# Kernel optimization log

Measured on AMD Instinct MI355X. Metric: run time of the kernel, lower is better.

Reference implementation:

```python
import jax, jax.numpy as jnp
import numpy as np

N = 10000        # nodes
E = 160000       # graph edges (avg degree 16)
EI = 100000      # interaction edges
EP = 50000       # positive interaction edges
EA = 50000       # a2b edges
H, D = 4, 128    # GAT heads, per-head (and per-layer) dim
F_IN, F_EDGE = 39, 27   # 17+19+3 node feats, 27 edge feats
EMB = 256
FCN_IN = F_IN + 3 * D + D  # 551: x stacked with 3 GAT outputs + GCN output

PARAM_SHAPES = []
for l, fin in enumerate([F_IN, D, D]):
    PARAM_SHAPES += [(f"gat{l}_W", (fin, H * D)), (f"gat{l}_We", (F_EDGE, H * D)),
                     (f"gat{l}_asrc", (H, D)), (f"gat{l}_adst", (H, D)),
                     (f"gat{l}_aedge", (H, D)), (f"gat{l}_b", (D,))]
PARAM_SHAPES += [("gcn_W", (D, D)), ("gcn_b", (D,))]
for nm, fi, hh, fo in [("fcn", FCN_IN, 1024, EMB), ("link", 2 * EMB + 2, 1024, 1),
                       ("a2b", 2 * EMB, 1024, 6), ("node", EMB, 1024, 16),
                       ("int", 2 * EMB + 2, 1024, 3)]:
    PARAM_SHAPES += [(f"{nm}_W1", (fi, hh)), (f"{nm}_b1", (hh,)),
                     (f"{nm}_g", (hh,)), (f"{nm}_be", (hh,)),
                     (f"{nm}_W2", (hh, fo)), (f"{nm}_b2", (fo,))]
PARAM_NAMES = [n for n, _ in PARAM_SHAPES]


def setup_inputs():
    ks = jax.random.split(jax.random.key(0), len(PARAM_SHAPES) + 10)
    inp = {
        "x": jax.random.normal(ks[0], (N, F_IN), jnp.float32),
        "edge_index": jax.random.randint(ks[1], (2, E), 0, N),
        "edge_attr": jax.random.normal(ks[2], (E, F_EDGE), jnp.float32),
        "interaction_edge_index_pos": jax.random.randint(ks[3], (2, EP), 0, N),
        "interaction_edge_index": jax.random.randint(ks[4], (2, EI), 0, N),
        "xyz_data": jax.random.normal(ks[5], (N, 3), jnp.float32),
        "vector_data": jax.random.normal(ks[6], (N, 3), jnp.float32),
        "a2b_index": jax.random.randint(ks[7], (2, EA), 0, N),
        "mask": jnp.zeros((1,), jnp.float32),  # only used by the (disabled) evolver path
    }
    for i, (name, shp) in enumerate(PARAM_SHAPES):
        if name.endswith("_g"):
            inp[name] = jnp.ones(shp, jnp.float32)        # BatchNorm gamma
        elif name.endswith(("_be", "_b", "_b1", "_b2")):
            inp[name] = jnp.zeros(shp, jnp.float32)       # biases / BN beta
        else:
            inp[name] = jax.random.normal(ks[10 + i], shp, jnp.float32) * 0.05
    return inp


def _bn(h, g, b, eps=1e-5):
    # BatchNorm1d in training mode: biased batch statistics over axis 0
    m = h.mean(0)
    v = ((h - m) ** 2).mean(0)
    return (h - m) * jax.lax.rsqrt(v + eps) * g + b


def _seg_softmax(logits, seg, n):
    m = jax.ops.segment_max(logits, seg, num_segments=n)
    e = jnp.exp(logits - m[seg])
    s = jax.ops.segment_sum(e, seg, num_segments=n)
    return e / (s[seg] + 1e-16)


def _cos(a, b, eps=1e-8):
    na = jnp.maximum(jnp.sqrt((a * a).sum(1)), eps)
    nb = jnp.maximum(jnp.sqrt((b * b).sum(1)), eps)
    return (a * b).sum(1) / (na * nb)


def _forward(x, edge_attr, xyz_data, vector_data, edge_index, iep, iei, a2b_index, params):
    p = dict(zip(PARAM_NAMES, params))
    n = x.shape[0]
    src, dst = edge_index[0], edge_index[1]
    loops = jnp.arange(n)
    # GATConv add_self_loops with fill_value='mean': per-node mean of incoming edge_attr
    cnt = jax.ops.segment_sum(jnp.ones(src.shape[0], x.dtype), dst, num_segments=n)
    loop_attr = jax.ops.segment_sum(edge_attr, dst, num_segments=n) / jnp.maximum(cnt, 1.0)[:, None]
    src_a = jnp.concatenate([src, loops])
    dst_a = jnp.concatenate([dst, loops])
    ea_a = jnp.concatenate([edge_attr, loop_attr], 0)

    def gat(xx, W, We, asrc, adst, aedge, b):
        h = (xx @ W).reshape(n, H, D)
        a_s = (h * asrc).sum(-1)                               # [n,H]
        a_d = (h * adst).sum(-1)                               # [n,H]
        a_e = ((ea_a @ We).reshape(-1, H, D) * aedge).sum(-1)  # [E',H]
        alpha = jax.nn.leaky_relu(a_s[src_a] + a_d[dst_a] + a_e, 0.2)
        alpha = _seg_softmax(alpha, dst_a, n)                  # softmax over incoming edges
        out = jax.ops.segment_sum(h[src_a] * alpha[:, :, None], dst_a, num_segments=n)
        return out.mean(1) + b                                 # concat=False -> mean over heads

    out = x
    steps = [x]
    for l in range(3):
        out = jax.nn.relu(gat(out, p[f"gat{l}_W"], p[f"gat{l}_We"], p[f"gat{l}_asrc"],
                              p[f"gat{l}_adst"], p[f"gat{l}_aedge"], p[f"gat{l}_b"]))
        steps.append(out)
    # GCNConv: self loops (weight 1) + symmetric normalization
    deg = jax.ops.segment_sum(jnp.ones(dst_a.shape[0], x.dtype), dst_a, num_segments=n)
    dinv = jnp.where(deg > 0, deg ** -0.5, 0.0)
    norm = dinv[src_a] * dinv[dst_a]
    hg = out @ p["gcn_W"]
    out = jax.ops.segment_sum(hg[src_a] * norm[:, None], dst_a, num_segments=n) + p["gcn_b"]
    steps.append(out)

    feat = jnp.concatenate(steps, 1)                           # [n, 551]
    h = jax.nn.relu(feat @ p["fcn_W1"] + p["fcn_b1"])
    h = _bn(h, p["fcn_g"], p["fcn_be"])
    emb = jax.nn.relu(h @ p["fcn_W2"] + p["fcn_b2"])           # [n, 256]

    def head(z, nm):
        hh = jax.nn.relu(z @ p[f"{nm}_W1"] + p[f"{nm}_b1"])
        hh = _bn(hh, p[f"{nm}_g"], p[f"{nm}_be"])
        return hh @ p[f"{nm}_W2"] + p[f"{nm}_b2"]

    def pair_feat(idx):
        z = jnp.concatenate([emb[idx[0]], emb[idx[1]]], 1)
        d = ((xyz_data[idx[0]] - xyz_data[idx[1]]) ** 2).sum(1)  # squared distance (no sqrt)
        a = _cos(vector_data[idx[0]], vector_data[idx[1]])
        return jnp.concatenate([z, d[:, None], a[:, None]], 1)

    link_preds = head(pair_feat(iei), "link")
    a2b_preds = head(jnp.concatenate([emb[a2b_index[0]], emb[a2b_index[1]]], 1), "a2b")
    node_preds = head(emb, "node")
    int_preds = head(pair_feat(iep), "int")
    return (link_preds, a2b_preds, node_preds, int_preds)


def reference(x, edge_index, edge_attr, interaction_edge_index_pos, interaction_edge_index,
              xyz_data, vector_data, a2b_index, mask,
              gat0_W, gat0_We, gat0_asrc, gat0_adst, gat0_aedge, gat0_b,
              gat1_W, gat1_We, gat1_asrc, gat1_adst, gat1_aedge, gat1_b,
              gat2_W, gat2_We, gat2_asrc, gat2_adst, gat2_aedge, gat2_b,
              gcn_W, gcn_b,
              fcn_W1, fcn_b1, fcn_g, fcn_be, fcn_W2, fcn_b2,
              link_W1, link_b1, link_g, link_be, link_W2, link_b2,
              a2b_W1, a2b_b1, a2b_g, a2b_be, a2b_W2, a2b_b2,
              node_W1, node_b1, node_g, node_be, node_W2, node_b2,
              int_W1, int_b1, int_g, int_be, int_W2, int_b2):
    loc = locals()
    params = tuple(loc[nm] for nm in PARAM_NAMES)
    return _forward(x, edge_attr, xyz_data, vector_data, edge_index,
                    interaction_edge_index_pos, interaction_edge_index, a2b_index, params)
```

## Files before the change

### kernel.cpp

```cpp
#include <hip/hip_runtime.h>
#include <hip/hip_bf16.h>
#include <cstdint>
#include <cstddef>

typedef __attribute__((ext_vector_type(8))) short bf16x8;
typedef __attribute__((ext_vector_type(4))) float f32x4;

__device__ inline float bf2f(unsigned short u) {
    union { float f; unsigned int i; } c; c.i = ((unsigned int)u) << 16; return c.f;
}
__device__ inline unsigned short f2b(float v) {
    __hip_bfloat16 h = __float2bfloat16(v);
    union { __hip_bfloat16 b; unsigned short u; } c; c.b = h; return c.u;
}

__device__ inline float wmax64(float v) {
    #pragma unroll
    for (int o = 32; o; o >>= 1) v = fmaxf(v, __shfl_xor(v, o));
    return v;
}
__device__ inline float wsum64(float v) {
    #pragma unroll
    for (int o = 32; o; o >>= 1) v += __shfl_xor(v, o);
    return v;
}

__global__ void k_count(const int* __restrict__ dst, int* __restrict__ indeg, int E_) {
    int e = blockIdx.x * 256 + threadIdx.x;
    if (e < E_) atomicAdd(&indeg[dst[e]], 1);
}

__global__ __launch_bounds__(1024) void k_scan(const int* __restrict__ indeg, int* __restrict__ coff, int nn) {
    __shared__ int part[1024];
    const int t = threadIdx.x;
    const int CH = (nn + 1023) >> 10;
    int loc[16];
    int s = 0;
    #pragma unroll
    for (int j = 0; j < 16; ++j) {
        if (j < CH) {
            int idx = t * CH + j;
            loc[j] = s;
            s += (idx < nn) ? indeg[idx] : 0;
        }
    }
    part[t] = s;
    __syncthreads();
    for (int o = 1; o < 1024; o <<= 1) {
        int v = (t >= o) ? part[t - o] : 0;
        __syncthreads();
        part[t] += v;
        __syncthreads();
    }
    const int base = (t > 0) ? part[t - 1] : 0;
    #pragma unroll
    for (int j = 0; j < 16; ++j) {
        if (j < CH) {
            int idx = t * CH + j;
            if (idx < nn) coff[idx] = base + loc[j];
        }
    }
    if (t == 1023) coff[nn] = part[1023];
}

__global__ void k_fill(const int* __restrict__ dst, const int* __restrict__ coff,
                       int* __restrict__ fill, int* __restrict__ ceid, int E_) {
    int e = blockIdx.x * 256 + threadIdx.x;
    if (e < E_) {
        int d = dst[e];
        int p = atomicAdd(&fill[d], 1);
        ceid[coff[d] + p] = e;
    }
}

__global__ void k_copy_x(const float* __restrict__ x, float* __restrict__ feat, int nn) {
    int t = blockIdx.x * 256 + threadIdx.x;
    if (t < nn * 39) feat[(size_t)(t / 39) * 551 + (t % 39)] = x[t];
}

__global__ __launch_bounds__(128) void k_loopattr(const float* __restrict__ ea, const int* __restrict__ coff,
                                                  const int* __restrict__ ceid, float* __restrict__ la, int nn) {
    int g = blockIdx.x * 4 + (threadIdx.x >> 5);
    int lane = threadIdx.x & 31;
    if (g >= nn || lane >= 27) return;
    int beg = coff[g], cnt = coff[g + 1] - beg;
    float v = 0.f;
    for (int e = 0; e < cnt; ++e) v += ea[(size_t)ceid[beg + e] * 27 + lane];
    la[(size_t)g * 27 + lane] = v / fmaxf((float)cnt, 1.f);
}

__global__ void k_wea(const float* __restrict__ We, const float* __restrict__ aedge, float* __restrict__ Wea) {
    int t = threadIdx.x;
    if (t >= 108) return;
    int f = t >> 2, hh = t & 3;
    float v = 0.f;
    for (int d = 0; d < 128; ++d) v += We[(size_t)f * 512 + hh * 128 + d] * aedge[hh * 128 + d];
    Wea[f * 4 + hh] = v;
}

__global__ void k_ae(const float* __restrict__ ea, const float* __restrict__ la,
                     const float* __restrict__ Wea, float* __restrict__ a_e, int E_, int nn) {
    int r = blockIdx.x * 256 + threadIdx.x;
    if (r >= E_ + nn) return;
    const float* src = (r < E_) ? (ea + (size_t)r * 27) : (la + (size_t)(r - E_) * 27);
    float o0 = 0, o1 = 0, o2 = 0, o3 = 0;
    #pragma unroll
    for (int f = 0; f < 27; ++f) {
        float xv = src[f];
        o0 += xv * Wea[f * 4 + 0];
        o1 += xv * Wea[f * 4 + 1];
        o2 += xv * Wea[f * 4 + 2];
        o3 += xv * Wea[f * 4 + 3];
    }
    a_e[(size_t)r * 4 + 0] = o0; a_e[(size_t)r * 4 + 1] = o1;
    a_e[(size_t)r * 4 + 2] = o2; a_e[(size_t)r * 4 + 3] = o3;
}

__global__ void k_asd(const float* __restrict__ h, const float* __restrict__ asrc,
                      const float* __restrict__ adst, float* __restrict__ a_s,
                      float* __restrict__ a_d, int nn) {
    int t = blockIdx.x * 256 + threadIdx.x;
    if (t >= nn * 4) return;
    int node = t >> 2, hh = t & 3;
    const float* hp = h + (size_t)node * 512 + hh * 128;
    float vs = 0.f, vd = 0.f;
    for (int d = 0; d < 128; ++d) {
        float xv = hp[d];
        vs += xv * asrc[hh * 128 + d];
        vd += xv * adst[hh * 128 + d];
    }
    a_s[t] = vs;
    a_d[t] = vd;
}

__global__ __launch_bounds__(64) void k_attn(
    const float* __restrict__ h, const float* __restrict__ a_s, const float* __restrict__ a_d,
    const float* __restrict__ a_e, const int* __restrict__ esrc,
    const int* __restrict__ coff, const int* __restrict__ ceid,
    const float* __restrict__ bvec, float* __restrict__ feat, int colofs, int E_) {
    const int i = blockIdx.x;
    const int lane = threadIdx.x;
    const int beg = coff[i];
    const int cnt = coff[i + 1] - beg;
    const int total = cnt + 1;
    const float d0 = a_d[i * 4 + 0], d1 = a_d[i * 4 + 1], d2 = a_d[i * 4 + 2], d3 = a_d[i * 4 + 3];
    float m0 = -1e30f, m1 = -1e30f, m2 = -1e30f, m3 = -1e30f;
    for (int e = lane; e < total; e += 64) {
        int eid, s;
        if (e < cnt) { eid = ceid[beg + e]; s = esrc[eid]; } else { eid = E_ + i; s = i; }
        float l0 = a_s[s * 4 + 0] + d0 + a_e[(size_t)eid * 4 + 0];
        float l1 = a_s[s * 4 + 1] + d1 + a_e[(size_t)eid * 4 + 1];
        float l2 = a_s[s * 4 + 2] + d2 + a_e[(size_t)eid * 4 + 2];
        float l3 = a_s[s * 4 + 3] + d3 + a_e[(size_t)eid * 4 + 3];
        l0 = l0 > 0.f ? l0 : 0.2f * l0;
        l1 = l1 > 0.f ? l1 : 0.2f * l1;
        l2 = l2 > 0.f ? l2 : 0.2f * l2;
        l3 = l3 > 0.f ? l3 : 0.2f * l3;
        m0 = fmaxf(m0, l0); m1 = fmaxf(m1, l1); m2 = fmaxf(m2, l2); m3 = fmaxf(m3, l3);
    }
    m0 = wmax64(m0); m1 = wmax64(m1); m2 = wmax64(m2); m3 = wmax64(m3);
    float s0 = 0, s1 = 0, s2 = 0, s3 = 0;
    for (int e = lane; e < total; e += 64) {
        int eid, s;
        if (e < cnt) { eid = ceid[beg + e]; s = esrc[eid]; } else { eid = E_ + i; s = i; }
        float l0 = a_s[s * 4 + 0] + d0 + a_e[(size_t)eid * 4 + 0];
        float l1 = a_s[s * 4 + 1] + d1 + a_e[(size_t)eid * 4 + 1];
        float l2 = a_s[s * 4 + 2] + d2 + a_e[(size_t)eid * 4 + 2];
        float l3 = a_s[s * 4 + 3] + d3 + a_e[(size_t)eid * 4 + 3];
        l0 = l0 > 0.f ? l0 : 0.2f * l0;
        l1 = l1 > 0.f ? l1 : 0.2f * l1;
        l2 = l2 > 0.f ? l2 : 0.2f * l2;
        l3 = l3 > 0.f ? l3 : 0.2f * l3;
        s0 += __expf(l0 - m0); s1 += __expf(l1 - m1);
        s2 += __expf(l2 - m2); s3 += __expf(l3 - m3);
    }
    s0 = wsum64(s0); s1 = wsum64(s1); s2 = wsum64(s2); s3 = wsum64(s3);
    const int myh = lane >> 4;
    const float mm = myh == 0 ? m0 : myh == 1 ? m1 : myh == 2 ? m2 : m3;
    const float sv = myh == 0 ? s0 : myh == 1 ? s1 : myh == 2 ? s2 : s3;
    const float dd = myh == 0 ? d0 : myh == 1 ? d1 : myh == 2 ? d2 : d3;
    const float iv = 1.f / (sv + 1e-16f);
    float acc[8] = {0, 0, 0, 0, 0, 0, 0, 0};
    for (int e = 0; e < total; ++e) {
        int eid, s;
        if (e < cnt) { eid = ceid[beg + e]; s = esrc[eid]; } else { eid = E_ + i; s = i; }
        float l = a_s[s * 4 + myh] + dd + a_e[(size_t)eid * 4 + myh];
        l = l > 0.f ? l : 0.2f * l;
        const float wgt = __expf(l - mm) * iv;
        const float4* hp = (const float4*)(h + (size_t)s * 512 + lane * 8);
        float4 x0 = hp[0], x1 = hp[1];
        acc[0] += wgt * x0.x; acc[1] += wgt * x0.y; acc[2] += wgt * x0.z; acc[3] += wgt * x0.w;
        acc[4] += wgt * x1.x; acc[5] += wgt * x1.y; acc[6] += wgt * x1.z; acc[7] += wgt * x1.w;
    }
    __shared__ float sh[512];
    #pragma unroll
    for (int j = 0; j < 8; ++j) sh[lane * 8 + j] = acc[j];
    __syncthreads();
    #pragma unroll
    for (int r = 0; r < 2; ++r) {
        int d = lane * 2 + r;
        float v = 0.25f * (sh[d] + sh[128 + d] + sh[256 + d] + sh[384 + d]) + bvec[d];
        feat[(size_t)i * 551 + colofs + d] = fmaxf(v, 0.f);
    }
}

__global__ __launch_bounds__(64) void k_gcn(const float* __restrict__ hg, const int* __restrict__ esrc,
    const int* __restrict__ coff, const int* __restrict__ ceid, const int* __restrict__ indeg,
    const float* __restrict__ bvec, float* __restrict__ feat) {
    const int i = blockIdx.x;
    const int lane = threadIdx.x;
    const int beg = coff[i];
    const int cnt = coff[i + 1] - beg;
    const float di = rsqrtf((float)(indeg[i] + 1));
    const int d = lane * 2;
    float acc0 = hg[(size_t)i * 128 + d] * di;
    float acc1 = hg[(size_t)i * 128 + d + 1] * di;
    for (int e = 0; e < cnt; ++e) {
        int eid = ceid[beg + e];
        int s = esrc[eid];
        float ds = rsqrtf((float)(indeg[s] + 1));
        acc0 += hg[(size_t)s * 128 + d] * ds;
        acc1 += hg[(size_t)s * 128 + d + 1] * ds;
    }
    feat[(size_t)i * 551 + 423 + d] = acc0 * di + bvec[d];
    feat[(size_t)i * 551 + 423 + d + 1] = acc1 * di + bvec[d + 1];
}

__global__ void k_pair(const int* __restrict__ idx, const float* __restrict__ xyz,
                       const float* __restrict__ vec, float* __restrict__ dv,
                       float* __restrict__ av, int P) {
    int p = blockIdx.x * 256 + threadIdx.x;
    if (p >= P) return;
    int i = idx[p], j = idx[P + p];
    float dx = xyz[i * 3] - xyz[j * 3];
    float dy = xyz[i * 3 + 1] - xyz[j * 3 + 1];
    float dz = xyz[i * 3 + 2] - xyz[j * 3 + 2];
    dv[p] = dx * dx + dy * dy + dz * dz;
    float a0 = vec[i * 3], a1 = vec[i * 3 + 1], a2 = vec[i * 3 + 2];
    float b0 = vec[j * 3], b1 = vec[j * 3 + 1], b2 = vec[j * 3 + 2];
    float na = fmaxf(sqrtf(a0 * a0 + a1 * a1 + a2 * a2), 1e-8f);
    float nb = fmaxf(sqrtf(b0 * b0 + b1 * b1 + b2 * b2), 1e-8f);
    av[p] = (a0 * b0 + a1 * b1 + a2 * b2) / (na * nb);
}

__global__ void k_stage_a(const float* __restrict__ src, int lds, int off,
                          unsigned short* __restrict__ dst, int ldd, int M, int K, int Mp) {
    int idx = blockIdx.x * 256 + threadIdx.x;
    if (idx >= Mp * ldd) return;
    int m = idx / ldd, k = idx - m * ldd;
    float v = (m < M && k < K) ? src[(size_t)m * lds + off + k] : 0.f;
    dst[idx] = f2b(v);
}

__global__ void k_conv_bt(const float* __restrict__ src, int ldn,
                          unsigned short* __restrict__ dst, int Kp, int K, int N, int Np) {
    int idx = blockIdx.x * 256 + threadIdx.x;
    if (idx >= Np * Kp) return;
    int nrow = idx / Kp, k = idx - nrow * Kp;
    float v = (nrow < N && k < K) ? src[(size_t)k * ldn + nrow] : 0.f;
    dst[idx] = f2b(v);
}

template<int OUT, bool RELU, bool BIAS>
__global__ __launch_bounds__(256) void gemm_mfma(
    const unsigned short* __restrict__ A, int lda,
    const unsigned short* __restrict__ Bt, int ldb,
    const float* __restrict__ bias,
    void* __restrict__ Cv, int ldc,
    int M, int N, int K) {
    const int t = threadIdx.x;
    const int lane = t & 63;
    const int wid = t >> 6;
    const int wm = wid >> 1, wn = wid & 1;
    const int bm0 = blockIdx.y * 128 + wm * 64;
    const int bn0 = blockIdx.x * 128 + wn * 64;
    const int r = lane & 15, g = lane >> 4;
    f32x4 acc[4][4] = {};
    const unsigned short* Ap = A + (size_t)(bm0 + r) * lda + 8 * g;
    const unsigned short* Bp = Bt + (size_t)(bn0 + r) * ldb + 8 * g;
    for (int k0 = 0; k0 < K; k0 += 32) {
        bf16x8 a[4], b[4];
        #pragma unroll
        for (int i = 0; i < 4; ++i) {
            a[i] = *(const bf16x8*)(Ap + (size_t)(i * 16) * lda + k0);
            b[i] = *(const bf16x8*)(Bp + (size_t)(i * 16) * ldb + k0);
        }
        #pragma unroll
        for (int i = 0; i < 4; ++i)
            #pragma unroll
            for (int j = 0; j < 4; ++j)
                acc[i][j] = __builtin_amdgcn_mfma_f32_16x16x32_bf16(a[i], b[j], acc[i][j], 0, 0, 0);
    }
    #pragma unroll
    for (int i = 0; i < 4; ++i) {
        #pragma unroll
        for (int reg = 0; reg < 4; ++reg) {
            const int row = bm0 + i * 16 + 4 * g + reg;
            if (row >= M) continue;
            #pragma unroll
            for (int j = 0; j < 4; ++j) {
                const int col = bn0 + j * 16 + r;
                if (col >= N) continue;
                float v = acc[i][j][reg];
                if constexpr (BIAS) v += bias[col];
                if constexpr (RELU) v = fmaxf(v, 0.f);
                if constexpr (OUT == 0) ((float*)Cv)[(size_t)row * ldc + col] = v;
                else ((unsigned short*)Cv)[(size_t)row * ldc + col] = f2b(v);
            }
        }
    }
}

__global__ __launch_bounds__(256) void k_stats1b(const unsigned short* __restrict__ Hm, int M, float* __restrict__ part) {
    const int b = blockIdx.x, t = threadIdx.x;
    const int chunk = (M + 255) / 256;
    const int r0 = b * chunk;
    const int r1 = min(M, r0 + chunk);
    float s[4] = {0, 0, 0, 0}, ss[4] = {0, 0, 0, 0};
    for (int r = r0; r < r1; ++r) {
        const ushort4 q = *(const ushort4*)(Hm + (size_t)r * 1024 + t * 4);
        float v0 = bf2f(q.x), v1 = bf2f(q.y), v2 = bf2f(q.z), v3 = bf2f(q.w);
        s[0] += v0; ss[0] += v0 * v0;
        s[1] += v1; ss[1] += v1 * v1;
        s[2] += v2; ss[2] += v2 * v2;
        s[3] += v3; ss[3] += v3 * v3;
    }
    #pragma unroll
    for (int j = 0; j < 4; ++j) {
        part[(size_t)b * 2048 + t * 4 + j] = s[j];
        part[(size_t)b * 2048 + 1024 + t * 4 + j] = ss[j];
    }
}

__global__ __launch_bounds__(256) void k_red1(const float* __restrict__ part, float* __restrict__ tmp,
                                              int NB, int nch) {
    const int c = blockIdx.x * 256 + threadIdx.x;
    const int ch = blockIdx.y;
    const int per = (NB + nch - 1) / nch;
    const int b0 = ch * per;
    const int b1 = min(NB, b0 + per);
    float s = 0.f;
    for (int b = b0; b < b1; ++b) s += part[(size_t)b * 2048 + c];
    tmp[(size_t)ch * 2048 + c] = s;
}
__global__ void k_red2(const float* __restrict__ tmp, float* __restrict__ mv, int M, int nch) {
    int c = blockIdx.x * 256 + threadIdx.x;
    if (c >= 1024) return;
    float s = 0.f, ss = 0.f;
    for (int ch = 0; ch < nch; ++ch) {
        s += tmp[(size_t)ch * 2048 + c];
        ss += tmp[(size_t)ch * 2048 + 1024 + c];
    }
    float m = s / (float)M;
    float v = ss / (float)M - m * m;
    mv[c] = m;
    mv[1024 + c] = fmaxf(v, 0.f);
}

__global__ __launch_bounds__(256) void k_fold(const float* __restrict__ W2, const float* __restrict__ g,
    const float* __restrict__ be, const float* __restrict__ b2, const float* __restrict__ mv,
    float* __restrict__ W2f, float* __restrict__ b2f, int NO) {
    const int c = blockIdx.x;
    const int t = threadIdx.x;
    __shared__ float red[256];
    float accb = 0.f;
    for (int k = t; k < 1024; k += 256) {
        float s = (1.f / sqrtf(mv[1024 + k] + 1e-5f)) * g[k];
        float wv = W2[(size_t)k * NO + c];
        W2f[(size_t)k * NO + c] = wv * s;
        accb += (be[k] - mv[k] * s) * wv;
    }
    red[t] = accb;
    __syncthreads();
    for (int o = 128; o; o >>= 1) {
        if (t < o) red[t] += red[t + o];
        __syncthreads();
    }
    if (t == 0) b2f[c] = b2[c] + red[0];
}

template<bool HASEX>
__global__ __launch_bounds__(256) void k_pairA(
    const unsigned short* __restrict__ u0, const unsigned short* __restrict__ u1,
    const float* __restrict__ b1, const float* __restrict__ W1ex,
    const int* __restrict__ idx, const float* __restrict__ dv, const float* __restrict__ av,
    int P, float* __restrict__ part) {
    const int b = blockIdx.x, t = threadIdx.x;
    const int chunk = (P + 1023) / 1024;
    const int r0 = b * chunk;
    const int r1 = min(P, r0 + chunk);
    const float4 bb = *(const float4*)(b1 + t * 4);
    float4 wd = make_float4(0, 0, 0, 0), wa = make_float4(0, 0, 0, 0);
    if constexpr (HASEX) {
        wd = *(const float4*)(W1ex + t * 4);
        wa = *(const float4*)(W1ex + 1024 + t * 4);
    }
    float s[4] = {0, 0, 0, 0}, ss[4] = {0, 0, 0, 0};
    for (int r = r0; r < r1; ++r) {
        const int i0 = idx[r], i1 = idx[P + r];
        const ushort4 q0 = *(const ushort4*)(u0 + (size_t)i0 * 1024 + t * 4);
        const ushort4 q1 = *(const ushort4*)(u1 + (size_t)i1 * 1024 + t * 4);
        float h[4];
        h[0] = bf2f(q0.x) + bf2f(q1.x) + bb.x;
        h[1] = bf2f(q0.y) + bf2f(q1.y) + bb.y;
        h[2] = bf2f(q0.z) + bf2f(q1.z) + bb.z;
        h[3] = bf2f(q0.w) + bf2f(q1.w) + bb.w;
        if constexpr (HASEX) {
            const float d = dv[r], a = av[r];
            h[0] += d * wd.x + a * wa.x;
            h[1] += d * wd.y + a * wa.y;
            h[2] += d * wd.z + a * wa.z;
            h[3] += d * wd.w + a * wa.w;
        }
        #pragma unroll
        for (int j = 0; j < 4; ++j) {
            float hv = fmaxf(h[j], 0.f);
            s[j] += hv; ss[j] += hv * hv;
        }
    }
    #pragma unroll
    for (int j = 0; j < 4; ++j) {
        part[(size_t)b * 2048 + t * 4 + j] = s[j];
        part[(size_t)b * 2048 + 1024 + t * 4 + j] = ss[j];
    }
}

template<int NO, bool HASEX>
__global__ __launch_bounds__(256) void k_pairB(
    const unsigned short* __restrict__ u0, const unsigned short* __restrict__ u1,
    const float* __restrict__ b1, const float* __restrict__ W1ex,
    const float* __restrict__ W2f, const float* __restrict__ b2f,
    const int* __restrict__ idx, const float* __restrict__ dv, const float* __restrict__ av,
    float* __restrict__ out, int P) {
    const int t = threadIdx.x;
    const int wid = t >> 6, lane = t & 63;
    const int row = blockIdx.x * 4 + wid;
    if (row >= P) return;
    const int i0 = idx[row], i1 = idx[P + row];
    const int k0 = lane * 16;
    float d = 0.f, a = 0.f;
    if constexpr (HASEX) { d = dv[row]; a = av[row]; }
    float acc[NO];
    #pragma unroll
    for (int no = 0; no < NO; ++no) acc[no] = 0.f;
    const unsigned short* p0 = u0 + (size_t)i0 * 1024 + k0;
    const unsigned short* p1 = u1 + (size_t)i1 * 1024 + k0;
    union { uint4 u; unsigned short us[8]; } qa0, qa1, qb0, qb1;
    qa0.u = *(const uint4*)(p0);
    qa1.u = *(const uint4*)(p0 + 8);
    qb0.u = *(const uint4*)(p1);
    qb1.u = *(const uint4*)(p1 + 8);
    #pragma unroll
    for (int j = 0; j < 16; ++j) {
        const int kk = k0 + j;
        float h = (j < 8 ? bf2f(qa0.us[j]) : bf2f(qa1.us[j - 8]))
                + (j < 8 ? bf2f(qb0.us[j]) : bf2f(qb1.us[j - 8]))
                + b1[kk];
        if constexpr (HASEX) h += d * W1ex[kk] + a * W1ex[1024 + kk];
        const float hv = fmaxf(h, 0.f);
        #pragma unroll
        for (int no = 0; no < NO; ++no) acc[no] += hv * W2f[(size_t)kk * NO + no];
    }
    #pragma unroll
    for (int no = 0; no < NO; ++no) {
        float v = acc[no];
        #pragma unroll
        for (int o = 32; o; o >>= 1) v += __shfl_down(v, o);
        if (lane == 0) out[(size_t)row * NO + no] = v + b2f[no];
    }
}

extern "C" void kernel_launch(void* const* d_in, const int* in_sizes, int n_in,
                              void* d_out, int out_size, void* d_ws, size_t ws_size,
                              hipStream_t stream) {
    (void)n_in; (void)out_size; (void)ws_size;
    const float* x     = (const float*)d_in[0];
    const int*   eidx  = (const int*)d_in[1];
    const float* eattr = (const float*)d_in[2];
    const int*   iep   = (const int*)d_in[3];
    const int*   iei   = (const int*)d_in[4];
    const float* xyz   = (const float*)d_in[5];
    const float* vecd  = (const float*)d_in[6];
    const int*   a2bi  = (const int*)d_in[7];

    const int n   = in_sizes[0] / 39;
    const int E_  = in_sizes[1] / 2;
    const int EPn = in_sizes[3] / 2;
    const int EIn = in_sizes[4] / 2;
    const int EAn = in_sizes[7] / 2;
    const int Mp  = (n + 127) & ~127;
    const int MB  = (n + 127) / 128;

    const float* gatW[3]  = {(const float*)d_in[9],  (const float*)d_in[15], (const float*)d_in[21]};
    const float* gatWe[3] = {(const float*)d_in[10], (const float*)d_in[16], (const float*)d_in[22]};
    const float* gatAs[3] = {(const float*)d_in[11], (const float*)d_in[17], (const float*)d_in[23]};
    const float* gatAd[3] = {(const float*)d_in[12], (const float*)d_in[18], (const float*)d_in[24]};
    const float* gatAe[3] = {(const float*)d_in[13], (const float*)d_in[19], (const float*)d_in[25]};
    const float* gatB[3]  = {(const float*)d_in[14], (const float*)d_in[20], (const float*)d_in[26]};
    const float* gcnW = (const float*)d_in[27];
    const float* gcnB = (const float*)d_in[28];
    const float* fcnW1 = (const float*)d_in[29];
    const float* fcnB1 = (const float*)d_in[30];
    const float* fcnG  = (const float*)d_in[31];
    const float* fcnBe = (const float*)d_in[32];
    const float* fcnW2 = (const float*)d_in[33];
    const float* fcnB2 = (const float*)d_in[34];

    struct HeadP { const float *W1, *b1, *g, *be, *W2, *b2; };
    HeadP hp[4];
    for (int hh = 0; hh < 4; ++hh) {
        int base = 35 + hh * 6;
        hp[hh] = {(const float*)d_in[base], (const float*)d_in[base + 1], (const float*)d_in[base + 2],
                  (const float*)d_in[base + 3], (const float*)d_in[base + 4], (const float*)d_in[base + 5]};
    }

    char* w = (char*)d_ws;
    size_t off = 0;
    auto alloc = [&](size_t bytes) -> void* {
        void* p = w + off;
        off = (off + bytes + 255) & ~(size_t)255;
        return p;
    };
    int* indeg   = (int*)alloc((size_t)n * 4);
    int* fill    = (int*)alloc((size_t)n * 4);
    int* coff    = (int*)alloc((size_t)(n + 1) * 4);
    int* ceid    = (int*)alloc((size_t)E_ * 4);
    float* lattr = (float*)alloc((size_t)n * 27 * 4);
    float* Wea   = (float*)alloc(27 * 4 * 4);
    float* a_e   = (float*)alloc((size_t)(E_ + n) * 4 * 4);
    float* a_s   = (float*)alloc((size_t)n * 4 * 4);
    float* a_d   = (float*)alloc((size_t)n * 4 * 4);
    float* part  = (float*)alloc((size_t)1024 * 2048 * 4);
    float* tmp   = (float*)alloc((size_t)32 * 2048 * 4);
    float* mv    = (float*)alloc(2048 * 4);
    float* W2f   = (float*)alloc((size_t)1024 * 256 * 4);
    float* b2f   = (float*)alloc(256 * 4);
    float* dlink = (float*)alloc((size_t)EIn * 4);
    float* alink = (float*)alloc((size_t)EIn * 4);
    float* dint  = (float*)alloc((size_t)EPn * 4);
    float* aint  = (float*)alloc((size_t)EPn * 4);
    float* feat  = (float*)alloc((size_t)n * 551 * 4);
    float* hbuf  = (float*)alloc((size_t)n * 512 * 4);
    unsigned short* Ab   = (unsigned short*)alloc((size_t)Mp * 576 * 2);
    unsigned short* hidb = (unsigned short*)alloc((size_t)Mp * 1024 * 2);
    unsigned short* embb = (unsigned short*)alloc((size_t)Mp * 256 * 2);
    unsigned short* u0b  = (unsigned short*)alloc((size_t)n * 1024 * 2);
    unsigned short* u1b  = (unsigned short*)alloc((size_t)n * 1024 * 2);
    unsigned short* btB  = (unsigned short*)alloc((size_t)1024 * 1024 * 2);

    hipMemsetAsync(indeg, 0, (size_t)n * 4, stream);
    hipMemsetAsync(fill, 0, (size_t)n * 4, stream);
    hipMemsetAsync(hidb + (size_t)n * 1024, 0, (size_t)(Mp - n) * 1024 * 2, stream);
    hipMemsetAsync(embb + (size_t)n * 256, 0, (size_t)(Mp - n) * 256 * 2, stream);

    const int NCH = 32;
    auto stats_finish = [&](int M, int NB) {
        dim3 g1(8, NCH);
        k_red1<<<g1, 256, 0, stream>>>(part, tmp, NB, NCH);
        k_red2<<<4, 256, 0, stream>>>(tmp, mv, M, NCH);
    };
    auto stageA = [&](const float* src, int lds, int colofs, int K, int Kp) {
        int tot = Mp * Kp;
        k_stage_a<<<(tot + 255) / 256, 256, 0, stream>>>(src, lds, colofs, Ab, Kp, n, K, Mp);
    };
    auto convBt = [&](const float* src, int ldn, int K, int Kp, int N, int Np) {
        int tot = Np * Kp;
        k_conv_bt<<<(tot + 255) / 256, 256, 0, stream>>>(src, ldn, btB, Kp, K, N, Np);
    };

    const int* dsta = eidx + E_;
    k_count<<<(E_ + 255) / 256, 256, 0, stream>>>(dsta, indeg, E_);
    k_scan<<<1, 1024, 0, stream>>>(indeg, coff, n);
    k_fill<<<(E_ + 255) / 256, 256, 0, stream>>>(dsta, coff, fill, ceid, E_);
    k_copy_x<<<((n * 39) + 255) / 256, 256, 0, stream>>>(x, feat, n);
    k_loopattr<<<(n + 3) / 4, 128, 0, stream>>>(eattr, coff, ceid, lattr, n);

    const int colofs_in[3] = {0, 39, 167};
    const int fin[3] = {39, 128, 128};
    const int finp[3] = {64, 128, 128};
    for (int l = 0; l < 3; ++l) {
        k_wea<<<1, 128, 0, stream>>>(gatWe[l], gatAe[l], Wea);
        stageA(feat, 551, colofs_in[l], fin[l], finp[l]);
        convBt(gatW[l], 512, fin[l], finp[l], 512, 512);
        dim3 g(4, MB);
        gemm_mfma<0, false, false><<<g, 256, 0, stream>>>(Ab, finp[l], btB, finp[l], nullptr, hbuf, 512, n, 512, finp[l]);
        k_ae<<<(E_ + n + 255) / 256, 256, 0, stream>>>(eattr, lattr, Wea, a_e, E_, n);
        k_asd<<<(n * 4 + 255) / 256, 256, 0, stream>>>(hbuf, gatAs[l], gatAd[l], a_s, a_d, n);
        k_attn<<<n, 64, 0, stream>>>(hbuf, a_s, a_d, a_e, eidx, coff, ceid, gatB[l], feat, 39 + 128 * l, E_);
    }
    {
        stageA(feat, 551, 295, 128, 128);
        convBt(gcnW, 128, 128, 128, 128, 128);
        dim3 g(1, MB);
        gemm_mfma<0, false, false><<<g, 256, 0, stream>>>(Ab, 128, btB, 128, nullptr, hbuf, 128, n, 128, 128);
        k_gcn<<<n, 64, 0, stream>>>(hbuf, eidx, coff, ceid, indeg, gcnB, feat);
    }
    {
        stageA(feat, 551, 0, 551, 576);
        convBt(fcnW1, 1024, 551, 576, 1024, 1024);
        dim3 g(8, MB);
        gemm_mfma<1, true, true><<<g, 256, 0, stream>>>(Ab, 576, btB, 576, fcnB1, hidb, 1024, n, 1024, 576);
        k_stats1b<<<256, 256, 0, stream>>>(hidb, n, part);
        stats_finish(n, 256);
        k_fold<<<256, 256, 0, stream>>>(fcnW2, fcnG, fcnBe, fcnB2, mv, W2f, b2f, 256);
        convBt(W2f, 256, 1024, 1024, 256, 256);
        dim3 g2(2, MB);
        gemm_mfma<1, true, true><<<g2, 256, 0, stream>>>(hidb, 1024, btB, 1024, b2f, embb, 256, n, 256, 1024);
    }
    k_pair<<<(EIn + 255) / 256, 256, 0, stream>>>(iei, xyz, vecd, dlink, alink, EIn);
    k_pair<<<(EPn + 255) / 256, 256, 0, stream>>>(iep, xyz, vecd, dint, aint, EPn);

    float* out = (float*)d_out;
    float* out_link = out;
    float* out_a2b  = out + (size_t)EIn;
    float* out_node = out_a2b + (size_t)EAn * 6;
    float* out_int  = out_node + (size_t)n * 16;

    const dim3 gu(8, MB);

    {
        convBt(hp[0].W1, 1024, 256, 256, 1024, 1024);
        gemm_mfma<1, false, false><<<gu, 256, 0, stream>>>(embb, 256, btB, 256, nullptr, u0b, 1024, n, 1024, 256);
        convBt(hp[0].W1 + (size_t)256 * 1024, 1024, 256, 256, 1024, 1024);
        gemm_mfma<1, false, false><<<gu, 256, 0, stream>>>(embb, 256, btB, 256, nullptr, u1b, 1024, n, 1024, 256);
        const float* W1ex = hp[0].W1 + (size_t)512 * 1024;
        k_pairA<true><<<1024, 256, 0, stream>>>(u0b, u1b, hp[0].b1, W1ex, iei, dlink, alink, EIn, part);
        stats_finish(EIn, 1024);
        k_fold<<<1, 256, 0, stream>>>(hp[0].W2, hp[0].g, hp[0].be, hp[0].b2, mv, W2f, b2f, 1);
        k_pairB<1, true><<<(EIn + 3) / 4, 256, 0, stream>>>(u0b, u1b, hp[0].b1, W1ex, W2f, b2f, iei, dlink, alink, out_link, EIn);
    }
    {
        convBt(hp[1].W1, 1024, 256, 256, 1024, 1024);
        gemm_mfma<1, false, false><<<gu, 256, 0, stream>>>(embb, 256, btB, 256, nullptr, u0b, 1024, n, 1024, 256);
        convBt(hp[1].W1 + (size_t)256 * 1024, 1024, 256, 256, 1024, 1024);
        gemm_mfma<1, false, false><<<gu, 256, 0, stream>>>(embb, 256, btB, 256, nullptr, u1b, 1024, n, 1024, 256);
        k_pairA<false><<<1024, 256, 0, stream>>>(u0b, u1b, hp[1].b1, nullptr, a2bi, nullptr, nullptr, EAn, part);
        stats_finish(EAn, 1024);
        k_fold<<<6, 256, 0, stream>>>(hp[1].W2, hp[1].g, hp[1].be, hp[1].b2, mv, W2f, b2f, 6);
        k_pairB<6, false><<<(EAn + 3) / 4, 256, 0, stream>>>(u0b, u1b, hp[1].b1, nullptr, W2f, b2f, a2bi, nullptr, nullptr, out_a2b, EAn);
    }
    {
        convBt(hp[2].W1, 1024, 256, 256, 1024, 1024);
        gemm_mfma<1, true, true><<<gu, 256, 0, stream>>>(embb, 256, btB, 256, hp[2].b1, hidb, 1024, n, 1024, 256);
        k_stats1b<<<256, 256, 0, stream>>>(hidb, n, part);
        stats_finish(n, 256);
        k_fold<<<16, 256, 0, stream>>>(hp[2].W2, hp[2].g, hp[2].be, hp[2].b2, mv, W2f, b2f, 16);
        convBt(W2f, 16, 1024, 1024, 16, 128);
        dim3 g2(1, MB);
        gemm_mfma<0, false, true><<<g2, 256, 0, stream>>>(hidb, 1024, btB, 1024, b2f, out_node, 16, n, 16, 1024);
    }
    {
        convBt(hp[3].W1, 1024, 256, 256, 1024, 1024);
        gemm_mfma<1, false, false><<<gu, 256, 0, stream>>>(embb, 256, btB, 256, nullptr, u0b, 1024, n, 1024, 256);
        convBt(hp[3].W1 + (size_t)256 * 1024, 1024, 256, 256, 1024, 1024);
        gemm_mfma<1, false, false><<<gu, 256, 0, stream>>>(embb, 256, btB, 256, nullptr, u1b, 1024, n, 1024, 256);
        const float* W1ex = hp[3].W1 + (size_t)512 * 1024;
        k_pairA<true><<<1024, 256, 0, stream>>>(u0b, u1b, hp[3].b1, W1ex, iep, dint, aint, EPn, part);
        stats_finish(EPn, 1024);
        k_fold<<<3, 256, 0, stream>>>(hp[3].W2, hp[3].g, hp[3].be, hp[3].b2, mv, W2f, b2f, 3);
        k_pairB<3, true><<<(EPn + 3) / 4, 256, 0, stream>>>(u0b, u1b, hp[3].b1, W1ex, W2f, b2f, iep, dint, aint, out_int, EPn);
    }
}
```

Baseline: 1.461 ms.

## Sort pair rows by source node to improve gather locality in pair heads

Before each pair head, a counting sort builds a permutation of pair rows grouped by first index (count, scan, fill into sid). k_pairA and k_pairB then process rows in that order, so consecutive rows reuse the same u0 row from cache. k_pairA is also unrolled by two to keep more gathers in flight. This adds three small kernels and two memsets per head. The nondeterministic atomic fill order may slightly change the float summation order of the statistics.

Result: slower. 1.582 ms (+8.3%).

```diff
diff --git a/kernel.cpp b/kernel.cpp
--- a/kernel.cpp
+++ b/kernel.cpp
@@ -383,7 +383,8 @@
 __global__ __launch_bounds__(256) void k_pairA(
     const unsigned short* __restrict__ u0, const unsigned short* __restrict__ u1,
     const float* __restrict__ b1, const float* __restrict__ W1ex,
-    const int* __restrict__ idx, const float* __restrict__ dv, const float* __restrict__ av,
+    const int* __restrict__ idx, const int* __restrict__ sid,
+    const float* __restrict__ dv, const float* __restrict__ av,
     int P, float* __restrict__ part) {
     const int b = blockIdx.x, t = threadIdx.x;
     const int chunk = (P + 1023) / 1024;
@@ -396,8 +397,42 @@
         wa = *(const float4*)(W1ex + 1024 + t * 4);
     }
     float s[4] = {0, 0, 0, 0}, ss[4] = {0, 0, 0, 0};
-    for (int r = r0; r < r1; ++r) {
-        const int i0 = idx[r], i1 = idx[P + r];
+    int r = r0;
+    for (; r + 1 < r1; r += 2) {
+        const int pA = sid[r], pB = sid[r + 1];
+        const int i0A = idx[pA], i1A = idx[P + pA];
+        const int i0B = idx[pB], i1B = idx[P + pB];
+        const ushort4 q0A = *(const ushort4*)(u0 + (size_t)i0A * 1024 + t * 4);
+        const ushort4 q1A = *(const ushort4*)(u1 + (size_t)i1A * 1024 + t * 4);
+        const ushort4 q0B = *(const ushort4*)(u0 + (size_t)i0B * 1024 + t * 4);
+        const ushort4 q1B = *(const ushort4*)(u1 + (size_t)i1B * 1024 + t * 4);
+        float hA[4], hB[4];
+        hA[0] = bf2f(q0A.x) + bf2f(q1A.x) + bb.x;
+        hA[1] = bf2f(q0A.y) + bf2f(q1A.y) + bb.y;
+        hA[2] = bf2f(q0A.z) + bf2f(q1A.z) + bb.z;
+        hA[3] = bf2f(q0A.w) + bf2f(q1A.w) + bb.w;
+        hB[0] = bf2f(q0B.x) + bf2f(q1B.x) + bb.x;
+        hB[1] = bf2f(q0B.y) + bf2f(q1B.y) + bb.y;
+        hB[2] = bf2f(q0B.z) + bf2f(q1B.z) + bb.z;
+        hB[3] = bf2f(q0B.w) + bf2f(q1B.w) + bb.w;
+        if constexpr (HASEX) {
+            const float dA = dv[pA], aA = av[pA];
+            const float dB = dv[pB], aB = av[pB];
+            hA[0] += dA * wd.x + aA * wa.x; hA[1] += dA * wd.y + aA * wa.y;
+            hA[2] += dA * wd.z + aA * wa.z; hA[3] += dA * wd.w + aA * wa.w;
+            hB[0] += dB * wd.x + aB * wa.x; hB[1] += dB * wd.y + aB * wa.y;
+            hB[2] += dB * wd.z + aB * wa.z; hB[3] += dB * wd.w + aB * wa.w;
+        }
+        #pragma unroll
+        for (int j = 0; j < 4; ++j) {
+            float hvA = fmaxf(hA[j], 0.f);
+            float hvB = fmaxf(hB[j], 0.f);
+            s[j] += hvA + hvB; ss[j] += hvA * hvA + hvB * hvB;
+        }
+    }
+    if (r < r1) {
+        const int p = sid[r];
+        const int i0 = idx[p], i1 = idx[P + p];
         const ushort4 q0 = *(const ushort4*)(u0 + (size_t)i0 * 1024 + t * 4);
         const ushort4 q1 = *(const ushort4*)(u1 + (size_t)i1 * 1024 + t * 4);
         float h[4];
@@ -406,11 +441,9 @@
         h[2] = bf2f(q0.z) + bf2f(q1.z) + bb.z;
         h[3] = bf2f(q0.w) + bf2f(q1.w) + bb.w;
         if constexpr (HASEX) {
-            const float d = dv[r], a = av[r];
-            h[0] += d * wd.x + a * wa.x;
-            h[1] += d * wd.y + a * wa.y;
-            h[2] += d * wd.z + a * wa.z;
-            h[3] += d * wd.w + a * wa.w;
+            const float d = dv[p], a = av[p];
+            h[0] += d * wd.x + a * wa.x; h[1] += d * wd.y + a * wa.y;
+            h[2] += d * wd.z + a * wa.z; h[3] += d * wd.w + a * wa.w;
         }
         #pragma unroll
         for (int j = 0; j < 4; ++j) {
@@ -430,12 +463,14 @@
     const unsigned short* __restrict__ u0, const unsigned short* __restrict__ u1,
     const float* __restrict__ b1, const float* __restrict__ W1ex,
     const float* __restrict__ W2f, const float* __restrict__ b2f,
-    const int* __restrict__ idx, const float* __restrict__ dv, const float* __restrict__ av,
+    const int* __restrict__ idx, const int* __restrict__ sid,
+    const float* __restrict__ dv, const float* __restrict__ av,
     float* __restrict__ out, int P) {
     const int t = threadIdx.x;
     const int wid = t >> 6, lane = t & 63;
-    const int row = blockIdx.x * 4 + wid;
-    if (row >= P) return;
+    const int srow = blockIdx.x * 4 + wid;
+    if (srow >= P) return;
+    const int row = sid[srow];
     const int i0 = idx[row], i1 = idx[P + row];
     const int k0 = lane * 16;
     float d = 0.f, a = 0.f;
@@ -525,6 +560,10 @@
     int* fill    = (int*)alloc((size_t)n * 4);
     int* coff    = (int*)alloc((size_t)(n + 1) * 4);
     int* ceid    = (int*)alloc((size_t)E_ * 4);
+    int* pcnt    = (int*)alloc((size_t)n * 4);
+    int* pfill   = (int*)alloc((size_t)n * 4);
+    int* poff    = (int*)alloc((size_t)(n + 1) * 4);
+    int* sid     = (int*)alloc((size_t)EIn * 4);
     float* lattr = (float*)alloc((size_t)n * 27 * 4);
     float* Wea   = (float*)alloc(27 * 4 * 4);
     float* a_e   = (float*)alloc((size_t)(E_ + n) * 4 * 4);
@@ -567,6 +606,13 @@
         int tot = Np * Kp;
         k_conv_bt<<<(tot + 255) / 256, 256, 0, stream>>>(src, ldn, btB, Kp, K, N, Np);
     };
+    auto sort_pairs = [&](const int* pidx, int P) {
+        hipMemsetAsync(pcnt, 0, (size_t)n * 4, stream);
+        hipMemsetAsync(pfill, 0, (size_t)n * 4, stream);
+        k_count<<<(P + 255) / 256, 256, 0, stream>>>(pidx, pcnt, P);
+        k_scan<<<1, 1024, 0, stream>>>(pcnt, poff, n);
+        k_fill<<<(P + 255) / 256, 256, 0, stream>>>(pidx, poff, pfill, sid, P);
+    };
 
     const int* dsta = eidx + E_;
     k_count<<<(E_ + 255) / 256, 256, 0, stream>>>(dsta, indeg, E_);
@@ -624,20 +670,22 @@
         convBt(hp[0].W1 + (size_t)256 * 1024, 1024, 256, 256, 1024, 1024);
         gemm_mfma<1, false, false><<<gu, 256, 0, stream>>>(embb, 256, btB, 256, nullptr, u1b, 1024, n, 1024, 256);
         const float* W1ex = hp[0].W1 + (size_t)512 * 1024;
-        k_pairA<true><<<1024, 256, 0, stream>>>(u0b, u1b, hp[0].b1, W1ex, iei, dlink, alink, EIn, part);
+        sort_pairs(iei, EIn);
+        k_pairA<true><<<1024, 256, 0, stream>>>(u0b, u1b, hp[0].b1, W1ex, iei, sid, dlink, alink, EIn, part);
         stats_finish(EIn, 1024);
         k_fold<<<1, 256, 0, stream>>>(hp[0].W2, hp[0].g, hp[0].be, hp[0].b2, mv, W2f, b2f, 1);
-        k_pairB<1, true><<<(EIn + 3) / 4, 256, 0, stream>>>(u0b, u1b, hp[0].b1, W1ex, W2f, b2f, iei, dlink, alink, out_link, EIn);
+        k_pairB<1, true><<<(EIn + 3) / 4, 256, 0, stream>>>(u0b, u1b, hp[0].b1, W1ex, W2f, b2f, iei, sid, dlink, alink, out_link, EIn);
     }
     {
         convBt(hp[1].W1, 1024, 256, 256, 1024, 1024);
         gemm_mfma<1, false, false><<<gu, 256, 0, stream>>>(embb, 256, btB, 256, nullptr, u0b, 1024, n, 1024, 256);
         convBt(hp[1].W1 + (size_t)256 * 1024, 1024, 256, 256, 1024, 1024);
         gemm_mfma<1, false, false><<<gu, 256, 0, stream>>>(embb, 256, btB, 256, nullptr, u1b, 1024, n, 1024, 256);
-        k_pairA<false><<<1024, 256, 0, stream>>>(u0b, u1b, hp[1].b1, nullptr, a2bi, nullptr, nullptr, EAn, part);
+        sort_pairs(a2bi, EAn);
+        k_pairA<false><<<1024, 256, 0, stream>>>(u0b, u1b, hp[1].b1, nullptr, a2bi, sid, nullptr, nullptr, EAn, part);
         stats_finish(EAn, 1024);
         k_fold<<<6, 256, 0, stream>>>(hp[1].W2, hp[1].g, hp[1].be, hp[1].b2, mv, W2f, b2f, 6);
-        k_pairB<6, false><<<(EAn + 3) / 4, 256, 0, stream>>>(u0b, u1b, hp[1].b1, nullptr, W2f, b2f, a2bi, nullptr, nullptr, out_a2b, EAn);
+        k_pairB<6, false><<<(EAn + 3) / 4, 256, 0, stream>>>(u0b, u1b, hp[1].b1, nullptr, W2f, b2f, a2bi, sid, nullptr, nullptr, out_a2b, EAn);
     }
     {
         convBt(hp[2].W1, 1024, 256, 256, 1024, 1024);
@@ -655,9 +703,10 @@
         convBt(hp[3].W1 + (size_t)256 * 1024, 1024, 256, 256, 1024, 1024);
         gemm_mfma<1, false, false><<<gu, 256, 0, stream>>>(embb, 256, btB, 256, nullptr, u1b, 1024, n, 1024, 256);
         const float* W1ex = hp[3].W1 + (size_t)512 * 1024;
-        k_pairA<true><<<1024, 256, 0, stream>>>(u0b, u1b, hp[3].b1, W1ex, iep, dint, aint, EPn, part);
+        sort_pairs(iep, EPn);
+        k_pairA<true><<<1024, 256, 0, stream>>>(u0b, u1b, hp[3].b1, W1ex, iep, sid, dint, aint, EPn, part);
         stats_finish(EPn, 1024);
         k_fold<<<3, 256, 0, stream>>>(hp[3].W2, hp[3].g, hp[3].be, hp[3].b2, mv, W2f, b2f, 3);
-        k_pairB<3, true><<<(EPn + 3) / 4, 256, 0, stream>>>(u0b, u1b, hp[3].b1, W1ex, W2f, b2f, iep, dint, aint, out_int, EPn);
-    }
-}
+        k_pairB<3, true><<<(EPn + 3) / 4, 256, 0, stream>>>(u0b, u1b, hp[3].b1, W1ex, W2f, b2f, iep, sid, dint, aint, out_int, EPn);
+    }
+}
```
